# Optimization experiments

Hardware: AMD Instinct MI355X
Metric: run time of the kernel (lower is better)

## Reference

```python
import jax, jax.numpy as jnp
import numpy as np

N, E, G = 4096, 65536, 64
C_IN, PE_DIM, H, L, HEADS, C_OUT = 64, 24, 128, 2, 4, 10
HD = H // HEADS


def setup_inputs() -> dict:
    key = jax.random.key(0)
    ks = iter(jax.random.split(key, 64))

    def nrm(shape, scale=0.05):
        return jax.random.normal(next(ks), shape, jnp.float32) * scale

    inp = {}
    inp["x"] = jax.random.normal(next(ks), (N, C_IN), jnp.float32)
    inp["lap_pe"] = jax.random.normal(next(ks), (N, 8), jnp.float32)
    inp["rw_pe"] = jax.random.normal(next(ks), (N, 16), jnp.float32)
    inp["edge_index"] = jax.random.randint(next(ks), (2, E), 0, N)
    inp["batch"] = jnp.sort(jax.random.randint(next(ks), (N,), 0, G))
    inp["Wp"] = nrm((C_IN + PE_DIM, H)); inp["bp"] = jnp.zeros((H,), jnp.float32)
    inp["gin_W1"] = nrm((L, H, H)); inp["gin_b1"] = jnp.zeros((L, H), jnp.float32)
    inp["gin_W2"] = nrm((L, H, H)); inp["gin_b2"] = jnp.zeros((L, H), jnp.float32)
    inp["bn1_g"] = jnp.ones((L, H), jnp.float32); inp["bn1_b"] = jnp.zeros((L, H), jnp.float32)
    inp["bn2_g"] = jnp.ones((L, H), jnp.float32); inp["bn2_b"] = jnp.zeros((L, H), jnp.float32)
    inp["bn3_g"] = jnp.ones((L, H), jnp.float32); inp["bn3_b"] = jnp.zeros((L, H), jnp.float32)
    inp["attn_in_w"] = nrm((L, H, 3 * H)); inp["attn_in_b"] = jnp.zeros((L, 3 * H), jnp.float32)
    inp["attn_out_w"] = nrm((L, H, H)); inp["attn_out_b"] = jnp.zeros((L, H), jnp.float32)
    inp["mlp_W1"] = nrm((L, H, 2 * H)); inp["mlp_b1"] = jnp.zeros((L, 2 * H), jnp.float32)
    inp["mlp_W2"] = nrm((L, 2 * H, H)); inp["mlp_b2"] = jnp.zeros((L, H), jnp.float32)
    inp["Wr1"] = nrm((H, H)); inp["br1"] = jnp.zeros((H,), jnp.float32)
    inp["Wr2"] = nrm((H, H)); inp["br2"] = jnp.zeros((H,), jnp.float32)
    inp["Wc"] = nrm((H, C_OUT)); inp["bc"] = jnp.zeros((C_OUT,), jnp.float32)
    return inp


def _bn(x, g, b):
    # BatchNorm1d over node dim, training-mode batch statistics (biased var)
    m = jnp.mean(x, axis=0)
    v = jnp.var(x, axis=0)
    return (x - m) * jax.lax.rsqrt(v + 1e-5) * g + b


def reference(x, lap_pe, rw_pe, edge_index, batch, Wp, bp,
              gin_W1, gin_b1, gin_W2, gin_b2,
              bn1_g, bn1_b, bn2_g, bn2_b, bn3_g, bn3_b,
              attn_in_w, attn_in_b, attn_out_w, attn_out_b,
              mlp_W1, mlp_b1, mlp_W2, mlp_b2,
              Wr1, br1, Wr2, br2, Wc, bc):
    pe = jnp.concatenate([lap_pe, rw_pe], axis=-1)          # [N, 24]
    h = jnp.concatenate([x, pe], axis=-1) @ Wp + bp         # [N, H]
    src, dst = edge_index[0], edge_index[1]
    scale = 1.0 / np.sqrt(HD)
    for l in range(L):
        # --- local GINConv: (1+eps)*x_i + sum_{j->i} x_j, eps=0, then 2-layer MLP ---
        agg = jax.ops.segment_sum(h[src], dst, num_segments=N)
        g = h + agg
        g = jax.nn.relu(g @ gin_W1[l] + gin_b1[l]) @ gin_W2[l] + gin_b2[l]
        g = _bn(g + h, bn1_g[l], bn1_b[l])                  # residual + norm1
        # --- global MHA; batch is NOT forwarded to GPSConv, so all N nodes form one dense graph ---
        qkv = h @ attn_in_w[l] + attn_in_b[l]               # [N, 3H]
        q, k, v = jnp.split(qkv, 3, axis=-1)
        q = q.reshape(N, HEADS, HD).transpose(1, 0, 2)      # [Hh, N, d]
        k = k.reshape(N, HEADS, HD).transpose(1, 0, 2)
        v = v.reshape(N, HEADS, HD).transpose(1, 0, 2)
        a = jax.nn.softmax(jnp.einsum('hnd,hmd->hnm', q, k) * scale, axis=-1)
        o = jnp.einsum('hnm,hmd->hnd', a, v).transpose(1, 0, 2).reshape(N, H)
        o = o @ attn_out_w[l] + attn_out_b[l]
        o = _bn(o + h, bn2_g[l], bn2_b[l])                  # residual + norm2
        # --- combine + FFN (channels -> 2*channels -> channels) + norm3 ---
        out = g + o
        m = jax.nn.relu(out @ mlp_W1[l] + mlp_b1[l]) @ mlp_W2[l] + mlp_b2[l]
        out = _bn(out + m, bn3_g[l], bn3_b[l])
        h = jax.nn.relu(out)                                # outer F.relu in GraphGPS
    pooled = jax.ops.segment_sum(h, batch, num_segments=G)  # global_add_pool
    r = jax.nn.relu(pooled @ Wr1 + br1)
    r = jax.nn.relu(r @ Wr2 + br2)                          # dropout(0.5) disabled (eval)
    return r @ Wc + bc                                      # [G, C_OUT]
```

## Files before the change

### kernel.cpp

```cpp
#include <hip/hip_runtime.h>
#include <hip/hip_bf16.h>
#include <math.h>

#define NN 4096
#define HH 128
#define EE 65536
#define GG 64
#define KSPLIT 8
#define KLEN (NN / KSPLIT)
#define SMEM_BYTES 14336

typedef unsigned short u16;
typedef unsigned int u32;
typedef __bf16 bf16x8 __attribute__((ext_vector_type(8)));
typedef float f32x4 __attribute__((ext_vector_type(4)));

__device__ inline u16 f2b(float f) {
  u32 u = __float_as_uint(f);
  u += 0x7FFFu + ((u >> 16) & 1u);
  return (u16)(u >> 16);
}
__device__ inline u32 pkbf2(float a, float b) {
  __hip_bfloat162 h = __float22bfloat162_rn(float2{a, b});
  u32 u; __builtin_memcpy(&u, &h, 4); return u;
}

struct TDesc { const float* src; int Ks, K, M, off; };
struct TPack { TDesc d[13]; };

__global__ __launch_bounds__(256) void transcount_k(TPack P, u16* __restrict__ dst,
    const int* __restrict__ ei, int* cnt) {
  if (blockIdx.x >= 1344) {
    int e = (blockIdx.x - 1344)*256 + threadIdx.x;
    atomicAdd(&cnt[ei[EE + e]], 1);
    return;
  }
  int idx = blockIdx.x * 256 + threadIdx.x;
  for (int i = 0; i < 13; i++) {
    int sz = P.d[i].K * P.d[i].M;
    if (idx < sz) {
      int m = idx / P.d[i].K;
      int k = idx - m * P.d[i].K;
      float v = (k < P.d[i].Ks) ? P.d[i].src[(size_t)k * P.d[i].M + m] : 0.f;
      dst[P.d[i].off + idx] = f2b(v);
      return;
    }
    idx -= sz;
  }
}

__global__ __launch_bounds__(256) void scan_k(const int* __restrict__ cnt,
    int* __restrict__ rowptr, int* __restrict__ cursor) {
  __shared__ int tot[256];
  int t = threadIdx.x;
  int base = t * 16;
  int loc[16]; int s = 0;
  #pragma unroll
  for (int i = 0; i < 16; i++) { loc[i] = s; s += cnt[base + i]; }
  tot[t] = s;
  __syncthreads();
  for (int off = 1; off < 256; off <<= 1) {
    int v = (t >= off) ? tot[t - off] : 0;
    __syncthreads();
    tot[t] += v;
    __syncthreads();
  }
  int excl = (t == 0) ? 0 : tot[t - 1];
  #pragma unroll
  for (int i = 0; i < 16; i++) {
    int p = excl + loc[i];
    rowptr[base + i] = p; cursor[base + i] = p;
  }
  if (t == 255) rowptr[NN] = excl + s;
}

__global__ __launch_bounds__(256) void aggcsr_k(const int* __restrict__ rowptr,
    const int* __restrict__ elist, const float* __restrict__ h,
    float* __restrict__ agg) {
  int d = blockIdx.x*2 + (threadIdx.x >> 7);
  int c = threadIdx.x & 127;
  int beg = rowptr[d], end = rowptr[d + 1];
  float acc = 0.f;
  for (int j = beg; j < end; j++)
    acc += h[(size_t)elist[j]*HH + c];
  agg[(size_t)d*HH + c] = acc;
}

struct GArgs {
  const float *A, *A2, *A3;
  const u16* Bt;
  const float* bias;
  float* C;
  const float *res, *res2;
  float* stats;
  const float *sbase, *pg1, *pb1, *pg2, *pb2;
  const float *opart, *lpart;
  u16 *qb, *kb, *vt;
  int K, M;
};

template <int ASTAGE, int EPI, int RELU>
__device__ void mgemm_dev(const GArgs& a, int bx, int by, char* smem) {
  char* Ab = smem;
  char* Bb = smem + 4096;
  float* affs = (float*)(smem + 12288);
  const int tid = threadIdx.x;
  const int n0 = bx * 32, m0 = by * 64;
  const int w = tid >> 6, lane = tid & 63;
  const int g = lane >> 4, li = lane & 15;
  const int wr = w >> 1, wc = w & 1;
  const int K = a.K, M = a.M;

  if (ASTAGE == 2) {
    int plane = tid >> 7, cc = tid & 127;
    const float* st = a.sbase + plane*256;
    const float* gg = plane ? a.pg2 : a.pg1;
    const float* bb = plane ? a.pb2 : a.pb1;
    float mean = st[cc] * (1.f/NN);
    float var  = st[128+cc] * (1.f/NN) - mean*mean;
    float s = rsqrtf(var + 1e-5f) * gg[cc];
    affs[plane*256 + cc]       = s;
    affs[plane*256 + 128 + cc] = bb[cc] - mean*s;
    __syncthreads();
  }

  f32x4 acc0 = {0,0,0,0}, acc1 = {0,0,0,0};
  const int arow = tid >> 3, akseg = (tid & 7) * 8;
  const int bcol = tid >> 2, bkseg = (tid & 3) * 16;

  for (int k0 = 0; k0 < K; k0 += 64) {
    {
      float4 a0 = {0,0,0,0}, a1 = {0,0,0,0};
      if (ASTAGE == 4) {
        int n = n0 + arow;
        if (k0 == 0) {
          a0 = *(const float4*)&a.A[(size_t)n*64 + akseg];
          a1 = *(const float4*)&a.A[(size_t)n*64 + akseg + 4];
        } else {
          if (akseg == 0)       { a0 = *(const float4*)&a.A2[(size_t)n*8];
                                  a1 = *(const float4*)&a.A2[(size_t)n*8 + 4]; }
          else if (akseg == 8)  { a0 = *(const float4*)&a.A3[(size_t)n*16];
                                  a1 = *(const float4*)&a.A3[(size_t)n*16 + 4]; }
          else if (akseg == 16) { a0 = *(const float4*)&a.A3[(size_t)n*16 + 8];
                                  a1 = *(const float4*)&a.A3[(size_t)n*16 + 12]; }
        }
      } else if (ASTAGE == 3) {
        int n = n0 + arow, c = k0 + akseg;
        int head = c >> 5, d0 = c & 31;
        float4 o0 = {0,0,0,0}, o1 = {0,0,0,0}; float L = 0.f;
        #pragma unroll
        for (int s = 0; s < KSPLIT; s++) {
          const float* ob = a.opart + ((size_t)(s*4+head)*NN + n)*32 + d0;
          float4 x0 = *(const float4*)ob, x1 = *(const float4*)(ob + 4);
          o0.x += x0.x; o0.y += x0.y; o0.z += x0.z; o0.w += x0.w;
          o1.x += x1.x; o1.y += x1.y; o1.z += x1.z; o1.w += x1.w;
          L += a.lpart[(size_t)(s*4+head)*NN + n];
        }
        float inv = 1.f / L;
        a0 = make_float4(o0.x*inv, o0.y*inv, o0.z*inv, o0.w*inv);
        a1 = make_float4(o1.x*inv, o1.y*inv, o1.z*inv, o1.w*inv);
      } else {
        const float* ap = a.A + (size_t)(n0 + arow) * K + k0 + akseg;
        a0 = *(const float4*)ap; a1 = *(const float4*)(ap + 4);
        if (ASTAGE == 1) {
          const float* p2 = a.A2 + (size_t)(n0 + arow) * K + k0 + akseg;
          float4 c0 = *(const float4*)p2, c1 = *(const float4*)(p2 + 4);
          a0.x += c0.x; a0.y += c0.y; a0.z += c0.z; a0.w += c0.w;
          a1.x += c1.x; a1.y += c1.y; a1.z += c1.z; a1.w += c1.w;
        } else if (ASTAGE == 2) {
          const float* p2 = a.A2 + (size_t)(n0 + arow) * K + k0 + akseg;
          float4 c0 = *(const float4*)p2, c1 = *(const float4*)(p2 + 4);
          const float* af = affs + k0 + akseg;
          float4 s1a = *(const float4*)af,         s1b = *(const float4*)(af + 4);
          float4 t1a = *(const float4*)(af + 128), t1b = *(const float4*)(af + 132);
          float4 s2a = *(const float4*)(af + 256), s2b = *(const float4*)(af + 260);
          float4 t2a = *(const float4*)(af + 384), t2b = *(const float4*)(af + 388);
          a0.x = a0.x*s1a.x + t1a.x + c0.x*s2a.x + t2a.x;
          a0.y = a0.y*s1a.y + t1a.y + c0.y*s2a.y + t2a.y;
          a0.z = a0.z*s1a.z + t1a.z + c0.z*s2a.z + t2a.z;
          a0.w = a0.w*s1a.w + t1a.w + c0.w*s2a.w + t2a.w;
          a1.x = a1.x*s1b.x + t1b.x + c1.x*s2b.x + t2b.x;
          a1.y = a1.y*s1b.y + t1b.y + c1.y*s2b.y + t2b.y;
          a1.z = a1.z*s1b.z + t1b.z + c1.z*s2b.z + t2b.z;
          a1.w = a1.w*s1b.w + t1b.w + c1.w*s2b.w + t2b.w;
        }
      }
      u16 t8[8] = {f2b(a0.x), f2b(a0.y), f2b(a0.z), f2b(a0.w),
                   f2b(a1.x), f2b(a1.y), f2b(a1.z), f2b(a1.w)};
      *(uint4*)(Ab + ((arow*128 + akseg*2) ^ ((arow & 7) << 4))) = *(uint4*)t8;
    }
    {
      const u16* bp = a.Bt + (size_t)(m0 + bcol) * K + k0 + bkseg;
      uint4 b0 = *(const uint4*)bp;
      uint4 b1 = *(const uint4*)(bp + 8);
      int ba = bcol*128 + bkseg*2;
      int sw = (bcol & 7) << 4;
      *(uint4*)(Bb + (ba ^ sw)) = b0;
      *(uint4*)(Bb + ((ba + 16) ^ sw)) = b1;
    }
    __syncthreads();
    int row = wr*16 + li;
    int cAl = wc*32 + li, cBl = cAl + 16;
    #pragma unroll
    for (int ck = 0; ck < 2; ck++) {
      bf16x8 af = *(const bf16x8*)(Ab + ((row*128 + ck*64 + g*16) ^ ((row & 7) << 4)));
      bf16x8 bf0 = *(const bf16x8*)(Bb + ((cAl*128 + ck*64 + g*16) ^ ((cAl & 7) << 4)));
      bf16x8 bf1 = *(const bf16x8*)(Bb + ((cBl*128 + ck*64 + g*16) ^ ((cBl & 7) << 4)));
      acc0 = __builtin_amdgcn_mfma_f32_16x16x32_bf16(af, bf0, acc0, 0, 0, 0);
      acc1 = __builtin_amdgcn_mfma_f32_16x16x32_bf16(af, bf1, acc1, 0, 0, 0);
    }
    __syncthreads();
  }

  const int colA = m0 + wc*32 + li, colB = colA + 16;
  const int colAl = wc*32 + li, colBl = colAl + 16;
  const int rbase = n0 + wr*16 + 4*g;

  if (EPI == 0) {
    float b0 = a.bias[colA], b1 = a.bias[colB];
    #pragma unroll
    for (int r = 0; r < 4; r++) {
      float v0 = acc0[r] + b0, v1 = acc1[r] + b1;
      if (RELU) { v0 = fmaxf(v0, 0.f); v1 = fmaxf(v1, 0.f); }
      a.C[(size_t)(rbase + r) * M + colA] = v0;
      a.C[(size_t)(rbase + r) * M + colB] = v1;
    }
  } else if (EPI == 1 || EPI == 3) {
    float b0 = a.bias[colA], b1 = a.bias[colB];
    float sA1=0, tA1=0, sA2=0, tA2=0, sB1=0, tB1=0, sB2=0, tB2=0;
    if (EPI == 3) {
      auto mk = [&](int col, float& s1, float& t1, float& s2, float& t2) {
        float m1 = a.sbase[col]*(1.f/NN), v1 = a.sbase[128+col]*(1.f/NN) - m1*m1;
        s1 = rsqrtf(v1 + 1e-5f) * a.pg1[col]; t1 = a.pb1[col] - m1*s1;
        float m2 = a.sbase[256+col]*(1.f/NN), v2 = a.sbase[384+col]*(1.f/NN) - m2*m2;
        s2 = rsqrtf(v2 + 1e-5f) * a.pg2[col]; t2 = a.pb2[col] - m2*s2;
      };
      mk(colA, sA1, tA1, sA2, tA2);
      mk(colB, sB1, tB1, sB2, tB2);
    }
    float s0 = 0, q0 = 0, s1 = 0, q1 = 0;
    #pragma unroll
    for (int r = 0; r < 4; r++) {
      int rw2 = rbase + r;
      float v0, v1;
      if (EPI == 1) {
        v0 = acc0[r] + b0 + a.res[(size_t)rw2 * 128 + colA];
        v1 = acc1[r] + b1 + a.res[(size_t)rw2 * 128 + colB];
      } else {
        v0 = acc0[r] + b0 + a.res[(size_t)rw2*128 + colA]*sA1 + tA1
                          + a.res2[(size_t)rw2*128 + colA]*sA2 + tA2;
        v1 = acc1[r] + b1 + a.res[(size_t)rw2*128 + colB]*sB1 + tB1
                          + a.res2[(size_t)rw2*128 + colB]*sB2 + tB2;
      }
      a.C[(size_t)rw2 * M + colA] = v0;
      a.C[(size_t)rw2 * M + colB] = v1;
      s0 += v0; q0 += v0*v0; s1 += v1; q1 += v1*v1;
    }
    s0 += __shfl_xor(s0, 16); s0 += __shfl_xor(s0, 32);
    q0 += __shfl_xor(q0, 16); q0 += __shfl_xor(q0, 32);
    s1 += __shfl_xor(s1, 16); s1 += __shfl_xor(s1, 32);
    q1 += __shfl_xor(q1, 16); q1 += __shfl_xor(q1, 32);
    float* sred = (float*)smem;
    if (lane < 16) {
      sred[wr*64 + colAl] = s0;  sred[128 + wr*64 + colAl] = q0;
      sred[wr*64 + colBl] = s1;  sred[128 + wr*64 + colBl] = q1;
    }
    __syncthreads();
    if (tid < 128) {
      int c = tid & 63, isq = tid >> 6;
      float v = sred[isq*128 + c] + sred[isq*128 + 64 + c];
      atomicAdd(&a.stats[isq*128 + m0 + c], v);
    }
  } else {
    const float QS = 0.17677669529663687f * 1.4426950408889634f;
    auto doq = [&](int col, f32x4 acc, float bb) {
      if (col < 128) {
        int hd = col >> 5, d = col & 31;
        #pragma unroll
        for (int r = 0; r < 4; r++)
          a.qb[((size_t)hd*NN + rbase + r)*32 + d] = f2b((acc[r] + bb) * QS);
      } else if (col < 256) {
        int hd = (col - 128) >> 5, d = col & 31;
        #pragma unroll
        for (int r = 0; r < 4; r++)
          a.kb[((size_t)hd*NN + rbase + r)*32 + d] = f2b(acc[r] + bb);
      } else {
        #pragma unroll
        for (int r = 0; r < 4; r++)
          a.vt[(size_t)(col - 256)*NN + rbase + r] = f2b(acc[r] + bb);
      }
    };
    doq(colA, acc0, a.bias[colA]);
    doq(colB, acc1, a.bias[colB]);
  }
}

template <int AS, int EP, int RE>
__global__ __launch_bounds__(256) void k_gemm(GArgs a) {
  extern __shared__ char smem[];
  mgemm_dev<AS, EP, RE>(a, blockIdx.x, blockIdx.y, smem);
}

__global__ __launch_bounds__(256) void k_qkv_gin1(GArgs qa, GArgs ga) {
  extern __shared__ char smem[];
  int b = blockIdx.x;
  if (b < 768) mgemm_dev<0,4,0>(qa, b & 127, b >> 7, smem);
  else { b -= 768; mgemm_dev<1,0,1>(ga, b & 127, b >> 7, smem); }
}

__global__ __launch_bounds__(256) void k_gin2_ao(GArgs g2, GArgs ao) {
  extern __shared__ char smem[];
  int b = blockIdx.x;
  if (b < 256) mgemm_dev<0,1,0>(g2, b & 127, b >> 7, smem);
  else { b -= 256; mgemm_dev<3,1,0>(ao, b & 127, b >> 7, smem); }
}

__global__ __launch_bounds__(256) void k_scat_inp(const int* __restrict__ ei,
    int* cursor, int* __restrict__ elist, GArgs ia) {
  extern __shared__ char smem[];
  int b = blockIdx.x;
  if (b < 256) {
    int e = b*256 + threadIdx.x;
    int d = ei[EE + e];
    int p = atomicAdd(&cursor[d], 1);
    elist[p] = ei[e];
  } else {
    b -= 256;
    mgemm_dev<4,0,0>(ia, b & 127, b >> 7, smem);
  }
}

__global__ __launch_bounds__(256) void bn3_k(
    const float* __restrict__ out3, const float* __restrict__ stats,
    const float* __restrict__ gamma, const float* __restrict__ beta,
    float* __restrict__ h, const int* __restrict__ batch,
    float* __restrict__ pooled, int dopool) {
  int idx = blockIdx.x*256 + threadIdx.x;
  int c = idx & 127;
  float mean = stats[c] * (1.f/NN);
  float var  = stats[128+c] * (1.f/NN) - mean*mean;
  float rs = rsqrtf(var + 1e-5f);
  float r = fmaxf((out3[idx] - mean) * rs * gamma[c] + beta[c], 0.f);
  if (dopool) atomicAdd(&pooled[batch[idx >> 7]*HH + c], r);
  else        h[idx] = r;
}

__global__ __launch_bounds__(512) void mfma_attn_k(
    const u16* __restrict__ qb, const u16* __restrict__ kb,
    const u16* __restrict__ vt, float* __restrict__ opart,
    float* __restrict__ lpart) {
  __shared__ __align__(16) u16 kbuf[2][2048];
  __shared__ __align__(16) u16 vbuf[2][2048];
  __shared__ __align__(16) u16 pbuf[8][1024];

  const int tid = threadIdx.x;
  const int w = tid >> 6, lane = tid & 63;
  const int g = lane >> 4, li = lane & 15;
  const int head = blockIdx.z;
  const int q0 = blockIdx.y * 128 + w * 16;
  const int j0 = blockIdx.x * KLEN;

  const bf16x8 qf = *reinterpret_cast<const bf16x8*>(
      qb + ((size_t)(head*NN) + q0 + li)*32 + g*8);

  const bool isK = tid < 256;
  const int kk = tid >> 2, dsg = (tid & 3) * 8;
  const int t2 = tid & 255;
  const int vd = t2 >> 3, vcs = (t2 & 7) ^ (vd & 7);
  const u16* kpan = kb + (size_t)head*NN*32;
  const u16* vrow_g = vt + (size_t)(head*32 + vd)*NN;

  f32x4 oacc0 = {0,0,0,0}, oacc1 = {0,0,0,0};
  const f32x4 zz = {0,0,0,0};
  float lsum = 0.f;
  char* pb = (char*)&pbuf[w][0];
  const int swz = (li & 7) << 4;

  {
    uint4 gld;
    if (isK) gld = *(const uint4*)(kpan + (size_t)(j0 + kk)*32 + dsg);
    else     gld = *(const uint4*)(vrow_g + j0 + vcs*8);
    if (isK) *(uint4*)(&kbuf[0][kk*32 + dsg]) = gld;
    else     *(uint4*)(&vbuf[0][vd*64 + vcs*8]) = gld;
  }
  __syncthreads();

  const int NSTEP = KLEN / 64;
  int cur = 0;
  for (int s = 0; s < NSTEP; s++) {
    int jt = j0 + s*64;
    bool pf = (s + 1 < NSTEP);
    uint4 gld = {0,0,0,0};
    if (pf) {
      if (isK) gld = *(const uint4*)(kpan + (size_t)(jt + 64 + kk)*32 + dsg);
      else     gld = *(const uint4*)(vrow_g + jt + 64 + vcs*8);
    }
    f32x4 st[4];
    #pragma unroll
    for (int t = 0; t < 4; t++) {
      bf16x8 kf = *(const bf16x8*)&kbuf[cur][(t*16 + li)*32 + g*8];
      st[t] = __builtin_amdgcn_mfma_f32_16x16x32_bf16(kf, qf, zz, 0, 0, 0);
    }
    #pragma unroll
    for (int t = 0; t < 4; t++) {
      float p0 = exp2f(st[t][0]), p1 = exp2f(st[t][1]);
      float p2 = exp2f(st[t][2]), p3 = exp2f(st[t][3]);
      lsum += p0 + p1 + p2 + p3;
      uint2 wv2;
      wv2.x = pkbf2(p0, p1);
      wv2.y = pkbf2(p2, p3);
      *(uint2*)(pb + ((li*128 + t*32 + g*8) ^ swz)) = wv2;
    }
    #pragma unroll
    for (int c = 0; c < 2; c++) {
      bf16x8 pa = *(const bf16x8*)(pb + ((li*128 + c*64 + g*16) ^ swz));
      int vs = ((c*4 + g) ^ (li & 7)) << 4;
      bf16x8 vb0 = *(const bf16x8*)((char*)vbuf[cur] + li*128 + vs);
      bf16x8 vb1 = *(const bf16x8*)((char*)vbuf[cur] + (16 + li)*128 + vs);
      oacc0 = __builtin_amdgcn_mfma_f32_16x16x32_bf16(pa, vb0, oacc0, 0, 0, 0);
      oacc1 = __builtin_amdgcn_mfma_f32_16x16x32_bf16(pa, vb1, oacc1, 0, 0, 0);
    }
    if (pf) {
      if (isK) *(uint4*)(&kbuf[cur ^ 1][kk*32 + dsg]) = gld;
      else     *(uint4*)(&vbuf[cur ^ 1][vd*64 + vcs*8]) = gld;
    }
    __syncthreads();
    cur ^= 1;
  }
  lsum += __shfl_xor(lsum, 16);
  lsum += __shfl_xor(lsum, 32);

  size_t b = (size_t)(blockIdx.x*4 + head)*NN + q0;
  #pragma unroll
  for (int r = 0; r < 4; r++) {
    size_t ob = (b + 4*g + r)*32;
    opart[ob + li]      = oacc0[r];
    opart[ob + 16 + li] = oacc1[r];
  }
  if (lane < 16) lpart[b + lane] = lsum;
}

__global__ __launch_bounds__(128) void head_k(
    const float* __restrict__ pooled,
    const float* __restrict__ Wr1, const float* __restrict__ br1,
    const float* __restrict__ Wr2, const float* __restrict__ br2,
    const float* __restrict__ Wc, const float* __restrict__ bc,
    float* __restrict__ out) {
  __shared__ float bufa[128], bufb[128];
  int g = blockIdx.x, c = threadIdx.x;
  bufa[c] = pooled[g*HH + c];
  __syncthreads();
  float acc = br1[c];
  #pragma unroll 8
  for (int k = 0; k < 128; k++) acc += bufa[k] * Wr1[k*128 + c];
  bufb[c] = fmaxf(acc, 0.f);
  __syncthreads();
  acc = br2[c];
  #pragma unroll 8
  for (int k = 0; k < 128; k++) acc += bufb[k] * Wr2[k*128 + c];
  bufa[c] = fmaxf(acc, 0.f);
  __syncthreads();
  if (c < 10) {
    acc = bc[c];
    #pragma unroll 8
    for (int k = 0; k < 128; k++) acc += bufa[k] * Wc[k*10 + c];
    out[g*10 + c] = acc;
  }
}

extern "C" void kernel_launch(void* const* d_in, const int* in_sizes, int n_in,
                              void* d_out, int out_size, void* d_ws, size_t ws_size,
                              hipStream_t stream) {
  const float* x      = (const float*)d_in[0];
  const float* lap    = (const float*)d_in[1];
  const float* rw     = (const float*)d_in[2];
  const int*   ei     = (const int*)d_in[3];
  const int*   batch  = (const int*)d_in[4];
  const float* Wp     = (const float*)d_in[5];
  const float* bp     = (const float*)d_in[6];
  const float* gin_W1 = (const float*)d_in[7];
  const float* gin_b1 = (const float*)d_in[8];
  const float* gin_W2 = (const float*)d_in[9];
  const float* gin_b2 = (const float*)d_in[10];
  const float* bn1_g  = (const float*)d_in[11];
  const float* bn1_b  = (const float*)d_in[12];
  const float* bn2_g  = (const float*)d_in[13];
  const float* bn2_b  = (const float*)d_in[14];
  const float* bn3_g  = (const float*)d_in[15];
  const float* bn3_b  = (const float*)d_in[16];
  const float* ain_w  = (const float*)d_in[17];
  const float* ain_b  = (const float*)d_in[18];
  const float* aout_w = (const float*)d_in[19];
  const float* aout_b = (const float*)d_in[20];
  const float* mlp_W1 = (const float*)d_in[21];
  const float* mlp_b1 = (const float*)d_in[22];
  const float* mlp_W2 = (const float*)d_in[23];
  const float* mlp_b2 = (const float*)d_in[24];
  const float* Wr1    = (const float*)d_in[25];
  const float* br1    = (const float*)d_in[26];
  const float* Wr2    = (const float*)d_in[27];
  const float* br2    = (const float*)d_in[28];
  const float* Wc     = (const float*)d_in[29];
  const float* bc     = (const float*)d_in[30];
  float* out = (float*)d_out;

  float* w = (float*)d_ws;
  float* h      = w + 0;
  float* agg    = w + 524288;
  float* gtmp   = w + 1048576;
  float* pre1   = w + 1572864;
  float* pre2   = w + 2097152;
  float* mlph   = w + 2621440;
  float* out3   = w + 3670016;
  float* opart  = w + 4194304;
  float* lpart  = w + 8388608;
  float* stats  = w + 8519680;
  float* pooled = w + 8521216;
  int*   cnt    = (int*)(w + 8529408);
  int*   rowptr = (int*)(w + 8533504);
  int*   cursor = (int*)(w + 8537608);
  int*   elist  = (int*)(w + 8541704);
  u16*   wts    = (u16*)(w + 8607240);
  u16*   qb     = (u16*)(w + 8779272);
  u16*   kb     = (u16*)(w + 9041416);
  u16*   vt     = (u16*)(w + 9303560);

  u16* wpt = wts;
  u16 *qkvWt[2], *g1t[2], *g2t[2], *aot[2], *m1t[2], *m2t[2];
  {
    int off = 16384;
    for (int l = 0; l < 2; l++) {
      qkvWt[l] = wts + off; off += 384*128;
      g1t[l]   = wts + off; off += 128*128;
      g2t[l]   = wts + off; off += 128*128;
      aot[l]   = wts + off; off += 128*128;
      m1t[l]   = wts + off; off += 256*128;
      m2t[l]   = wts + off; off += 128*256;
    }
  }
  TPack tp;
  {
    int ti = 0, toff = 0;
    auto addm = [&](const float* s, int Ks, int Kd, int Md) {
      tp.d[ti].src = s; tp.d[ti].Ks = Ks; tp.d[ti].K = Kd; tp.d[ti].M = Md;
      tp.d[ti].off = toff; toff += Kd * Md; ti++;
    };
    addm(Wp, 88, 128, 128);
    for (int l = 0; l < 2; l++) {
      addm(ain_w + l*HH*384, 128, 128, 384);
      addm(gin_W1 + l*HH*HH, 128, 128, 128);
      addm(gin_W2 + l*HH*HH, 128, 128, 128);
      addm(aout_w + l*HH*HH, 128, 128, 128);
      addm(mlp_W1 + l*HH*256, 128, 128, 256);
      addm(mlp_W2 + l*256*HH, 256, 256, 128);
    }
  }

  auto GA = [&](const float* A, const float* A2, const float* A3, const u16* Bt,
                const float* bias, float* C, const float* res, const float* res2,
                float* st, const float* sb, const float* g1, const float* b1,
                const float* g2, const float* b2, const float* op, const float* lp,
                u16* q, u16* k, u16* v, int K, int M) {
    GArgs a; a.A=A; a.A2=A2; a.A3=A3; a.Bt=Bt; a.bias=bias; a.C=C; a.res=res;
    a.res2=res2; a.stats=st; a.sbase=sb; a.pg1=g1; a.pb1=b1; a.pg2=g2; a.pb2=b2;
    a.opart=op; a.lpart=lp; a.qb=q; a.kb=k; a.vt=v; a.K=K; a.M=M; return a;
  };

  hipMemsetAsync(stats, 0, 13824*sizeof(float), stream);
  transcount_k<<<1600, 256, 0, stream>>>(tp, wts, ei, cnt);
  scan_k<<<1, 256, 0, stream>>>(cnt, rowptr, cursor);
  k_scat_inp<<<512, 256, SMEM_BYTES, stream>>>(ei, cursor, elist,
      GA(x, lap, rw, wpt, bp, h, nullptr, nullptr, nullptr, nullptr,
         nullptr, nullptr, nullptr, nullptr, nullptr, nullptr,
         nullptr, nullptr, nullptr, 128, 128));

  for (int l = 0; l < 2; l++) {
    float* st1 = stats + l*768;
    float* st2 = st1 + 256;
    float* st3 = st1 + 512;

    aggcsr_k<<<NN/2, 256, 0, stream>>>(rowptr, elist, h, agg);

    k_qkv_gin1<<<1024, 256, SMEM_BYTES, stream>>>(
        GA(h, nullptr, nullptr, qkvWt[l], ain_b + l*384, nullptr, nullptr,
           nullptr, nullptr, nullptr, nullptr, nullptr, nullptr, nullptr,
           nullptr, nullptr, qb, kb, vt, 128, 384),
        GA(h, agg, nullptr, g1t[l], gin_b1 + l*HH, gtmp, nullptr, nullptr,
           nullptr, nullptr, nullptr, nullptr, nullptr, nullptr,
           nullptr, nullptr, nullptr, nullptr, nullptr, 128, 128));

    mfma_attn_k<<<dim3(KSPLIT, NN/128, 4), 512, 0, stream>>>(qb, kb, vt, opart, lpart);

    k_gin2_ao<<<512, 256, SMEM_BYTES, stream>>>(
        GA(gtmp, nullptr, nullptr, g2t[l], gin_b2 + l*HH, pre1, h, nullptr,
           st1, nullptr, nullptr, nullptr, nullptr, nullptr,
           nullptr, nullptr, nullptr, nullptr, nullptr, 128, 128),
        GA(nullptr, nullptr, nullptr, aot[l], aout_b + l*HH, pre2, h, nullptr,
           st2, nullptr, nullptr, nullptr, nullptr, nullptr,
           opart, lpart, nullptr, nullptr, nullptr, 128, 128));

    k_gemm<2,0,1><<<dim3(128,4), 256, SMEM_BYTES, stream>>>(
        GA(pre1, pre2, nullptr, m1t[l], mlp_b1 + l*256, mlph, nullptr, nullptr,
           nullptr, st1, bn1_g + l*HH, bn1_b + l*HH, bn2_g + l*HH, bn2_b + l*HH,
           nullptr, nullptr, nullptr, nullptr, nullptr, 128, 256));
    k_gemm<0,3,0><<<dim3(128,2), 256, SMEM_BYTES, stream>>>(
        GA(mlph, nullptr, nullptr, m2t[l], mlp_b2 + l*HH, out3, pre1, pre2,
           st3, st1, bn1_g + l*HH, bn1_b + l*HH, bn2_g + l*HH, bn2_b + l*HH,
           nullptr, nullptr, nullptr, nullptr, nullptr, 256, 128));
    bn3_k<<<NN*HH/256, 256, 0, stream>>>(out3, st3, bn3_g + l*HH, bn3_b + l*HH,
                                         h, batch, pooled, l == 1);
  }

  head_k<<<GG, 128, 0, stream>>>(pooled, Wr1, br1, Wr2, br2, Wc, bc, out);
}
```

Baseline: 215.1 us.

## Halve attention block to 4 waves, each handling two query tiles

The attention kernel now runs 256 threads per block instead of 512, and each wave processes two 16-row query tiles (rows q0 and q0+64) against the same staged K/V tile. This lets each K/V fragment read from shared memory serve two MFMA chains and removes the K-thread/V-thread split, since every thread now loads one K vector and one V vector. s_setprio hints are added around the MFMA sections so the scheduler favours matrix work. In exchange there are fewer waves per block and more registers per wave, which may reduce latency hiding.

```diff
diff --git a/kernel.cpp b/kernel.cpp
--- a/kernel.cpp
+++ b/kernel.cpp
@@ -345,13 +345,13 @@
   else        h[idx] = r;
 }
 
-__global__ __launch_bounds__(512) void mfma_attn_k(
+__global__ __launch_bounds__(256) void mfma_attn_k(
     const u16* __restrict__ qb, const u16* __restrict__ kb,
     const u16* __restrict__ vt, float* __restrict__ opart,
     float* __restrict__ lpart) {
   __shared__ __align__(16) u16 kbuf[2][2048];
   __shared__ __align__(16) u16 vbuf[2][2048];
-  __shared__ __align__(16) u16 pbuf[8][1024];
+  __shared__ __align__(16) u16 pbuf[4][1024];
 
   const int tid = threadIdx.x;
   const int w = tid >> 6, lane = tid & 63;
@@ -360,28 +360,28 @@
   const int q0 = blockIdx.y * 128 + w * 16;
   const int j0 = blockIdx.x * KLEN;
 
-  const bf16x8 qf = *reinterpret_cast<const bf16x8*>(
+  const bf16x8 qfA = *reinterpret_cast<const bf16x8*>(
       qb + ((size_t)(head*NN) + q0 + li)*32 + g*8);
-
-  const bool isK = tid < 256;
-  const int kk = tid >> 2, dsg = (tid & 3) * 8;
-  const int t2 = tid & 255;
-  const int vd = t2 >> 3, vcs = (t2 & 7) ^ (vd & 7);
+  const bf16x8 qfB = *reinterpret_cast<const bf16x8*>(
+      qb + ((size_t)(head*NN) + q0 + 64 + li)*32 + g*8);
+
+  const int vd = tid >> 3;
+  const int vcs = (tid & 7) ^ (vd & 7);
   const u16* kpan = kb + (size_t)head*NN*32;
   const u16* vrow_g = vt + (size_t)(head*32 + vd)*NN;
 
-  f32x4 oacc0 = {0,0,0,0}, oacc1 = {0,0,0,0};
+  f32x4 oA0 = {0,0,0,0}, oA1 = {0,0,0,0};
+  f32x4 oB0 = {0,0,0,0}, oB1 = {0,0,0,0};
   const f32x4 zz = {0,0,0,0};
-  float lsum = 0.f;
+  float lsA = 0.f, lsB = 0.f;
   char* pb = (char*)&pbuf[w][0];
   const int swz = (li & 7) << 4;
 
   {
-    uint4 gld;
-    if (isK) gld = *(const uint4*)(kpan + (size_t)(j0 + kk)*32 + dsg);
-    else     gld = *(const uint4*)(vrow_g + j0 + vcs*8);
-    if (isK) *(uint4*)(&kbuf[0][kk*32 + dsg]) = gld;
-    else     *(uint4*)(&vbuf[0][vd*64 + vcs*8]) = gld;
+    uint4 kv = *(const uint4*)(kpan + (size_t)j0*32 + tid*8);
+    uint4 vv = *(const uint4*)(vrow_g + j0 + vcs*8);
+    *((uint4*)kbuf[0] + tid) = kv;
+    *((uint4*)vbuf[0] + tid) = vv;
   }
   __syncthreads();
 
@@ -390,54 +390,78 @@
   for (int s = 0; s < NSTEP; s++) {
     int jt = j0 + s*64;
     bool pf = (s + 1 < NSTEP);
-    uint4 gld = {0,0,0,0};
+    uint4 kv = {0,0,0,0}, vv = {0,0,0,0};
     if (pf) {
-      if (isK) gld = *(const uint4*)(kpan + (size_t)(jt + 64 + kk)*32 + dsg);
-      else     gld = *(const uint4*)(vrow_g + jt + 64 + vcs*8);
-    }
-    f32x4 st[4];
+      kv = *(const uint4*)(kpan + (size_t)(jt + 64)*32 + tid*8);
+      vv = *(const uint4*)(vrow_g + jt + 64 + vcs*8);
+    }
     #pragma unroll
-    for (int t = 0; t < 4; t++) {
-      bf16x8 kf = *(const bf16x8*)&kbuf[cur][(t*16 + li)*32 + g*8];
-      st[t] = __builtin_amdgcn_mfma_f32_16x16x32_bf16(kf, qf, zz, 0, 0, 0);
-    }
-    #pragma unroll
-    for (int t = 0; t < 4; t++) {
-      float p0 = exp2f(st[t][0]), p1 = exp2f(st[t][1]);
-      float p2 = exp2f(st[t][2]), p3 = exp2f(st[t][3]);
-      lsum += p0 + p1 + p2 + p3;
-      uint2 wv2;
-      wv2.x = pkbf2(p0, p1);
-      wv2.y = pkbf2(p2, p3);
-      *(uint2*)(pb + ((li*128 + t*32 + g*8) ^ swz)) = wv2;
-    }
-    #pragma unroll
-    for (int c = 0; c < 2; c++) {
-      bf16x8 pa = *(const bf16x8*)(pb + ((li*128 + c*64 + g*16) ^ swz));
-      int vs = ((c*4 + g) ^ (li & 7)) << 4;
-      bf16x8 vb0 = *(const bf16x8*)((char*)vbuf[cur] + li*128 + vs);
-      bf16x8 vb1 = *(const bf16x8*)((char*)vbuf[cur] + (16 + li)*128 + vs);
-      oacc0 = __builtin_amdgcn_mfma_f32_16x16x32_bf16(pa, vb0, oacc0, 0, 0, 0);
-      oacc1 = __builtin_amdgcn_mfma_f32_16x16x32_bf16(pa, vb1, oacc1, 0, 0, 0);
+    for (int qq = 0; qq < 2; qq++) {
+      const bf16x8 qf = qq ? qfB : qfA;
+      f32x4 st[4];
+      __builtin_amdgcn_s_setprio(1);
+      #pragma unroll
+      for (int t = 0; t < 4; t++) {
+        bf16x8 kf = *(const bf16x8*)&kbuf[cur][(t*16 + li)*32 + g*8];
+        st[t] = __builtin_amdgcn_mfma_f32_16x16x32_bf16(kf, qf, zz, 0, 0, 0);
+      }
+      __builtin_amdgcn_s_setprio(0);
+      float lloc = 0.f;
+      #pragma unroll
+      for (int t = 0; t < 4; t++) {
+        float p0 = exp2f(st[t][0]), p1 = exp2f(st[t][1]);
+        float p2 = exp2f(st[t][2]), p3 = exp2f(st[t][3]);
+        lloc += p0 + p1 + p2 + p3;
+        uint2 wv2;
+        wv2.x = pkbf2(p0, p1);
+        wv2.y = pkbf2(p2, p3);
+        *(uint2*)(pb + ((li*128 + t*32 + g*8) ^ swz)) = wv2;
+      }
+      if (qq) lsB += lloc; else lsA += lloc;
+      __builtin_amdgcn_s_setprio(1);
+      #pragma unroll
+      for (int c = 0; c < 2; c++) {
+        bf16x8 pa = *(const bf16x8*)(pb + ((li*128 + c*64 + g*16) ^ swz));
+        int vs = ((c*4 + g) ^ (li & 7)) << 4;
+        bf16x8 vb0 = *(const bf16x8*)((char*)vbuf[cur] + li*128 + vs);
+        bf16x8 vb1 = *(const bf16x8*)((char*)vbuf[cur] + (16 + li)*128 + vs);
+        if (qq) {
+          oB0 = __builtin_amdgcn_mfma_f32_16x16x32_bf16(pa, vb0, oB0, 0, 0, 0);
+          oB1 = __builtin_amdgcn_mfma_f32_16x16x32_bf16(pa, vb1, oB1, 0, 0, 0);
+        } else {
+          oA0 = __builtin_amdgcn_mfma_f32_16x16x32_bf16(pa, vb0, oA0, 0, 0, 0);
+          oA1 = __builtin_amdgcn_mfma_f32_16x16x32_bf16(pa, vb1, oA1, 0, 0, 0);
+        }
+      }
+      __builtin_amdgcn_s_setprio(0);
     }
     if (pf) {
-      if (isK) *(uint4*)(&kbuf[cur ^ 1][kk*32 + dsg]) = gld;
-      else     *(uint4*)(&vbuf[cur ^ 1][vd*64 + vcs*8]) = gld;
+      *((uint4*)kbuf[cur ^ 1] + tid) = kv;
+      *((uint4*)vbuf[cur ^ 1] + tid) = vv;
     }
     __syncthreads();
     cur ^= 1;
   }
-  lsum += __shfl_xor(lsum, 16);
-  lsum += __shfl_xor(lsum, 32);
+  lsA += __shfl_xor(lsA, 16);
+  lsA += __shfl_xor(lsA, 32);
+  lsB += __shfl_xor(lsB, 16);
+  lsB += __shfl_xor(lsB, 32);
 
   size_t b = (size_t)(blockIdx.x*4 + head)*NN + q0;
+  size_t b2 = b + 64;
   #pragma unroll
   for (int r = 0; r < 4; r++) {
     size_t ob = (b + 4*g + r)*32;
-    opart[ob + li]      = oacc0[r];
-    opart[ob + 16 + li] = oacc1[r];
-  }
-  if (lane < 16) lpart[b + lane] = lsum;
+    opart[ob + li]      = oA0[r];
+    opart[ob + 16 + li] = oA1[r];
+    size_t ob2 = (b2 + 4*g + r)*32;
+    opart[ob2 + li]      = oB0[r];
+    opart[ob2 + 16 + li] = oB1[r];
+  }
+  if (lane < 16) {
+    lpart[b + lane]  = lsA;
+    lpart[b2 + lane] = lsB;
+  }
 }
 
 __global__ __launch_bounds__(128) void head_k(
@@ -589,7 +613,7 @@
            nullptr, nullptr, nullptr, nullptr, nullptr, nullptr,
            nullptr, nullptr, nullptr, nullptr, nullptr, 128, 128));
 
-    mfma_attn_k<<<dim3(KSPLIT, NN/128, 4), 512, 0, stream>>>(qb, kb, vt, opart, lpart);
+    mfma_attn_k<<<dim3(KSPLIT, NN/128, 4), 256, 0, stream>>>(qb, kb, vt, opart, lpart);
 
     k_gin2_ao<<<512, 256, SMEM_BYTES, stream>>>(
         GA(gtmp, nullptr, nullptr, g2t[l], gin_b2 + l*HH, pre1, h, nullptr,
```

Measured after the change: 194.5 us. 9.6% less time.
